# Kernel optimization log

Measured on AMD Instinct MI355X. Metric: run time of the kernel, lower is better.

Reference implementation:

```python
import jax, jax.numpy as jnp
import numpy as np

B, S, D_IN, D_OUT, RANK = 4, 2048, 4096, 4096, 32
BLOCK = 16
Q_MAX = 7.0  # INT4: 2**(4-1) - 1


def quantize_uniform(x, block_size=BLOCK, q_max=Q_MAX):
    """Block-wise symmetric fake-quantize (round-to-nearest, clamp)."""
    orig_shape = x.shape
    xf = x.reshape(-1, block_size)
    amax = jnp.clip(jnp.max(jnp.abs(xf), axis=-1, keepdims=True), 1e-12, None)
    scale = amax / q_max
    xq = jnp.clip(jnp.round(xf / scale), -q_max, q_max) * scale
    return xq.reshape(orig_shape)


def setup_inputs() -> dict:
    key = jax.random.key(0)
    ks = jax.random.split(key, 7)
    x = jax.random.normal(ks[0], (B, S, D_IN), jnp.float32)
    smooth_scale = jax.random.uniform(ks[1], (D_IN,), jnp.float32, 0.5, 2.0)
    w_quantized = jax.random.normal(ks[2], (D_OUT, D_IN), jnp.float32) * 0.02
    lora_a = jax.random.normal(ks[3], (RANK, D_IN), jnp.float32) * 0.02
    lora_b = jax.random.normal(ks[4], (D_OUT, RANK), jnp.float32) * 0.02
    w_sparse = jax.random.normal(ks[5], (D_OUT, D_IN), jnp.float32) * 0.02
    bias = jax.random.normal(ks[6], (D_OUT,), jnp.float32) * 0.02
    return {"x": x, "smooth_scale": smooth_scale, "w_quantized": w_quantized,
            "lora_a": lora_a, "lora_b": lora_b, "w_sparse": w_sparse, "bias": bias}


def reference(x, smooth_scale, w_quantized, lora_a, lora_b, w_sparse, bias):
    # smoothing (SmoothQuant-style per-channel scale)
    x_smoothed = x * smooth_scale                      # [B,S,Din]
    # block-wise INT4 fake-quantize of the smoothed activations
    x_q = quantize_uniform(x_smoothed)                 # [B,S,Din]
    # quantized main path
    base_out = jnp.einsum('bsi,oi->bso', x_q, w_quantized)
    # low-rank SVD error-correction path
    svd_out = jnp.einsum('bsr,or->bso',
                         jnp.einsum('bsi,ri->bsr', x_smoothed, lora_a),
                         lora_b)
    # sparse-outlier path (unsmoothed x)
    sparse_out = jnp.einsum('bsi,oi->bso', x, w_sparse)
    return base_out + svd_out + sparse_out + bias
```

## Files before the change

kernel.cpp:

```cpp
#include <hip/hip_runtime.h>
#include <stdint.h>

typedef float  f32x4  __attribute__((ext_vector_type(4)));
typedef __bf16 bf16x8 __attribute__((ext_vector_type(8)));
typedef unsigned int   u32;
typedef unsigned short u16;
typedef unsigned long long u64;
typedef u32 u32x4 __attribute__((ext_vector_type(4)));

#define M_TOT 8192
#define N_TOT 4096
#define K_DIN 4096
#define RANK  32
#define KCAT  8320
#define NTILE 130
#define KLAST 8256

__device__ __forceinline__ u16 f2bf(float f) {
  union { float f; u32 u; } v; v.f = f;
  u32 r = v.u + 0x7fffu + ((v.u >> 16) & 1u);
  return (u16)(r >> 16);
}

__global__ void prep_b_k(const float* __restrict__ wq, const float* __restrict__ wsp,
                         const float* __restrict__ lb, const float* __restrict__ la,
                         const float* __restrict__ ss,
                         u16* __restrict__ Bb, u16* __restrict__ asb) {
  const int b = blockIdx.x;
  const int tid = threadIdx.x;
  if (b < 32768) {
    const float* src = (b < 16384) ? wq : wsp;
    const int colofs = (b < 16384) ? 0 : K_DIN;
    const int i = (b & 16383) * 256 + tid;
    f32x4 v = ((const f32x4*)src)[i];
    int r = i >> 10, c = (i & 1023) * 4;
    alignas(8) u16 o[4] = { f2bf(v[0]), f2bf(v[1]), f2bf(v[2]), f2bf(v[3]) };
    *(u64*)(Bb + (size_t)r * KCAT + colofs + c) = *(const u64*)o;
  } else if (b < 32896) {
    const int i = (b - 32768) * 256 + tid;
    f32x4 v = ((const f32x4*)lb)[i];
    int row = i >> 3, c = (i & 7) * 4;
    alignas(8) u16 o[4] = { f2bf(v[0]), f2bf(v[1]), f2bf(v[2]), f2bf(v[3]) };
    u16* rp = Bb + (size_t)row * KCAT;
    *(u64*)(rp + 2 * K_DIN + c) = *(const u64*)o;
    u16* zp = rp + 2 * K_DIN + RANK + (i & 7) * 12;
    *(u64*)(zp + 0) = 0; *(u64*)(zp + 4) = 0; *(u64*)(zp + 8) = 0;
  } else {
    const int i = (b - 32896) * 256 + tid;
    f32x4 v = ((const f32x4*)la)[i];
    f32x4 s = ((const f32x4*)ss)[i & 1023];
    f32x4 p = v * s;
    alignas(8) u16 o[4] = { f2bf(p[0]), f2bf(p[1]), f2bf(p[2]), f2bf(p[3]) };
    *(u64*)(asb + 4 * (size_t)i) = *(const u64*)o;
  }
}

__global__ void prep_x_k(const float* __restrict__ x, const float* __restrict__ ss,
                         u16* __restrict__ Ab) {
  int m = blockIdx.x;
  int t = threadIdx.x;
  const f32x4* xp = (const f32x4*)(x + (size_t)m * K_DIN + t * 16);
  const f32x4* sp = (const f32x4*)(ss + t * 16);
  float xs[16];
  alignas(16) u16 rb[16], qb[16];
  float amax = 0.0f;
  #pragma unroll
  for (int i = 0; i < 4; ++i) {
    f32x4 a = xp[i], s = sp[i];
    #pragma unroll
    for (int j = 0; j < 4; ++j) {
      float xr = a[j];
      float v  = xr * s[j];
      xs[i*4+j] = v;
      amax = fmaxf(amax, fabsf(v));
      rb[i*4+j] = f2bf(xr);
    }
  }
  amax = fmaxf(amax, 1e-12f);
  float scale = amax / 7.0f;
  #pragma unroll
  for (int i = 0; i < 16; ++i) {
    float r = rintf(xs[i] / scale);
    r = fminf(7.0f, fmaxf(-7.0f, r));
    qb[i] = f2bf(r * scale);
  }
  u16* qo = Ab + (size_t)m * KCAT + t * 16;
  ((u32x4*)qo)[0] = ((const u32x4*)qb)[0];
  ((u32x4*)qo)[1] = ((const u32x4*)qb)[1];
  u16* ro = qo + K_DIN;
  ((u32x4*)ro)[0] = ((const u32x4*)rb)[0];
  ((u32x4*)ro)[1] = ((const u32x4*)rb)[1];
}

__global__ __launch_bounds__(256)
void lora_t_mfma_k(u16* __restrict__ Ab, const u16* __restrict__ asb) {
  const int wave = threadIdx.x >> 6;
  const int lane = threadIdx.x & 63;
  const int lr = lane & 15, lg = lane >> 4;
  const int m0 = blockIdx.x * 64 + wave * 16;
  f32x4 acc0 = {}, acc1 = {};
  for (int k0 = 0; k0 < K_DIN; k0 += 32) {
    bf16x8 a  = *(const bf16x8*)(Ab + (size_t)(m0 + lr) * KCAT + K_DIN + k0 + lg * 8);
    bf16x8 b0 = *(const bf16x8*)(asb + (size_t)lr        * K_DIN + k0 + lg * 8);
    bf16x8 b1 = *(const bf16x8*)(asb + (size_t)(16 + lr) * K_DIN + k0 + lg * 8);
    acc0 = __builtin_amdgcn_mfma_f32_16x16x32_bf16(a, b0, acc0, 0, 0, 0);
    acc1 = __builtin_amdgcn_mfma_f32_16x16x32_bf16(a, b1, acc1, 0, 0, 0);
  }
  #pragma unroll
  for (int j = 0; j < 4; ++j) {
    const int row = m0 + lg * 4 + j;
    Ab[(size_t)row * KCAT + 2 * K_DIN + lr]      = f2bf(acc0[j]);
    Ab[(size_t)row * KCAT + 2 * K_DIN + 16 + lr] = f2bf(acc1[j]);
  }
  const int zr = blockIdx.x * 64 + (threadIdx.x >> 2);
  u16* zp = Ab + (size_t)zr * KCAT + 2 * K_DIN + RANK + (threadIdx.x & 3) * 24;
  #pragma unroll
  for (int q = 0; q < 6; ++q) *(u64*)(zp + q * 4) = 0;
}

__device__ __forceinline__ void gld_lds16(const u16* g, u16* l) {
  __builtin_amdgcn_global_load_lds((const __attribute__((address_space(1))) u32*)g,
                                   (__attribute__((address_space(3))) u32*)l,
                                   16, 0, 0);
}

#define BAR()  __builtin_amdgcn_s_barrier()
#define VMW6() asm volatile("s_waitcnt vmcnt(6)" ::: "memory")
#define BUF1 32768

#define LDA(bufel, mh) do { _Pragma("unroll")                                        \
  for (int m_ = 0; m_ < 4; ++m_) {                                                   \
    Ar[m_][0] = *(const bf16x8*)(smem + (bufel) + aoff + ((mh)*4+m_)*1024 + blk0);    \
    Ar[m_][1] = *(const bf16x8*)(smem + (bufel) + aoff + ((mh)*4+m_)*1024 + blk1);    \
  } } while (0)

#define LDB(bufel, nh) do { _Pragma("unroll")                                        \
  for (int n_ = 0; n_ < 2; ++n_) {                                                   \
    Br[(nh)*2+n_][0] = *(const bf16x8*)(smem + (bufel) + boff + ((nh)*2+n_)*1024 + blk0); \
    Br[(nh)*2+n_][1] = *(const bf16x8*)(smem + (bufel) + boff + ((nh)*2+n_)*1024 + blk1); \
  } } while (0)

#define MMQ2(mh) do {                                                                \
  __builtin_amdgcn_s_setprio(1);                                                     \
  _Pragma("unroll")                                                                  \
  for (int m_ = 0; m_ < 4; ++m_) { _Pragma("unroll")                                 \
    for (int n_ = 0; n_ < 4; ++n_) {                                                 \
      acc[(mh)*4+m_][n_] = __builtin_amdgcn_mfma_f32_16x16x32_bf16(                  \
          Ar[m_][0], Br[n_][0], acc[(mh)*4+m_][n_], 0, 0, 0);                        \
      acc[(mh)*4+m_][n_] = __builtin_amdgcn_mfma_f32_16x16x32_bf16(                  \
          Ar[m_][1], Br[n_][1], acc[(mh)*4+m_][n_], 0, 0, 0);                        \
    } }                                                                              \
  __builtin_amdgcn_s_setprio(0);                                                     \
} while (0)

__global__ __launch_bounds__(512, 2)
void gemm8_k(const u16* __restrict__ Ab, const u16* __restrict__ Bb,
             const float* __restrict__ bias, float* __restrict__ out) {
  extern __shared__ u16 smem[];
  const int tid  = threadIdx.x;
  const int wave = tid >> 6;
  const int lane = tid & 63;
  const int lr = lane & 15, lg = lane >> 4;
  const int wm = wave >> 2, wn = wave & 3;

  const int wg  = blockIdx.x;
  const int swz = (wg & 7) * 64 + (wg >> 3);
  const int m0 = (swz >> 4) * 256;
  const int n0 = (swz & 15) * 256;

  const int aoff = wm * 8192 + lr * 64;
  const int boff = 16384 + wn * 4096 + lr * 64;
  const int e7   = lr & 7;
  const int blk0 = ((0 + lg) ^ e7) * 8;
  const int blk1 = ((4 + lg) ^ e7) * 8;

  const int srow = tid >> 3;
  const int scol = ((tid & 7) ^ (srow & 7)) * 8;
  const int woff = wave * 512;

  const u16* aRow = Ab + (size_t)(m0 + srow) * KCAT + scol;
  const u16* bRow = Bb + (size_t)(n0 + srow) * KCAT + scol;
  u16* dstA0 = smem + woff;
  u16* dstB0 = smem + 16384 + woff;

  bf16x8 Ar[4][2], Br[4][2];
  f32x4 acc[8][4] = {};

  auto stgA = [&](int kof, int h, int bufel) {
    u16* dst = dstA0 + bufel + h * 8192;
    gld_lds16(aRow + (size_t)(h * 128) * KCAT + kof, dst);
    gld_lds16(aRow + (size_t)(h * 128 + 64) * KCAT + kof, dst + 4096);
  };
  auto stgB = [&](int kof, int h, int bufel) {
    u16* dst = dstB0 + bufel + h * 8192;
    gld_lds16(bRow + (size_t)(h * 128) * KCAT + kof, dst);
    gld_lds16(bRow + (size_t)(h * 128 + 64) * KCAT + kof, dst + 4096);
  };

  stgA(0, 0, 0);     stgA(0, 1, 0);
  stgB(0, 0, 0);     stgB(0, 1, 0);
  stgB(64, 0, BUF1); stgB(64, 1, BUF1);
  stgA(64, 0, BUF1);
  VMW6();
  BAR();

  for (int it = 0; it < NTILE / 2; ++it) {
    const int ka = it * 128;
    int c2 = ka + 128, c3 = ka + 192;
    if (c2 > KLAST) c2 = KLAST;
    if (c3 > KLAST) c3 = KLAST;
    LDA(0, 0); LDB(0, 0); LDB(0, 1);
    stgA(ka + 64, 1, BUF1);
    BAR(); MMQ2(0); BAR();
    LDA(0, 1);
    stgB(c2, 0, 0); stgB(c2, 1, 0); stgA(c2, 0, 0);
    BAR(); MMQ2(1);
    VMW6();
    BAR();
    LDA(BUF1, 0); LDB(BUF1, 0); LDB(BUF1, 1);
    stgA(c2, 1, 0);
    BAR(); MMQ2(0); BAR();
    LDA(BUF1, 1);
    stgB(c3, 0, BUF1); stgB(c3, 1, BUF1); stgA(c3, 0, BUF1);
    BAR(); MMQ2(1);
    VMW6();
    BAR();
  }

  float bv[4];
  #pragma unroll
  for (int n = 0; n < 4; ++n) bv[n] = bias[n0 + wn * 64 + n * 16 + lr];
  #pragma unroll
  for (int m = 0; m < 8; ++m) {
    const int row = m0 + wm * 128 + m * 16 + lg * 4;
    #pragma unroll
    for (int n = 0; n < 4; ++n) {
      const int col = n0 + wn * 64 + n * 16 + lr;
      float* op = out + (size_t)row * N_TOT + col;
      op[0 * (size_t)N_TOT] = acc[m][n][0] + bv[n];
      op[1 * (size_t)N_TOT] = acc[m][n][1] + bv[n];
      op[2 * (size_t)N_TOT] = acc[m][n][2] + bv[n];
      op[3 * (size_t)N_TOT] = acc[m][n][3] + bv[n];
    }
  }
}

extern "C" void kernel_launch(void* const* d_in, const int* in_sizes, int n_in,
                              void* d_out, int out_size, void* d_ws, size_t ws_size,
                              hipStream_t stream) {
  const float* x    = (const float*)d_in[0];
  const float* ss   = (const float*)d_in[1];
  const float* wq   = (const float*)d_in[2];
  const float* la   = (const float*)d_in[3];
  const float* lb   = (const float*)d_in[4];
  const float* wsp  = (const float*)d_in[5];
  const float* bias = (const float*)d_in[6];
  float* out = (float*)d_out;

  uint8_t* w = (uint8_t*)d_ws;
  u16* Ab  = (u16*)w;  w += (size_t)M_TOT * KCAT * 2;
  u16* Bb  = (u16*)w;  w += (size_t)N_TOT * KCAT * 2;
  u16* asb = (u16*)w;

  prep_b_k<<<33024, 256, 0, stream>>>(wq, wsp, lb, la, ss, Bb, asb);
  prep_x_k<<<M_TOT, 256, 0, stream>>>(x, ss, Ab);
  lora_t_mfma_k<<<M_TOT / 64, 256, 0, stream>>>(Ab, asb);

  hipFuncSetAttribute((const void*)gemm8_k,
                      hipFuncAttributeMaxDynamicSharedMemorySize, 131072);
  gemm8_k<<<dim3((N_TOT / 256) * (M_TOT / 256)), 512, 131072, stream>>>(
      Ab, Bb, bias, out);
}
```

Baseline: 608.5 us.

## Split MFMA phases into quarter-tiles to interleave LDS reads and global stages

Splits each half-tile MFMA block into two quarter blocks indexed by n-half. The B fragment loads and global-to-LDS stages are spread between these finer phases, with the second m-half walked in reversed n order so the resident B registers are reused. The aim is better overlap of LDS reads and memory issue with matrix work in the ping-pong schedule. The cost is twice as many barriers per iteration, which may add synchronisation stalls.

```diff
diff --git a/kernel.cpp b/kernel.cpp
--- a/kernel.cpp
+++ b/kernel.cpp
@@ -140,15 +140,15 @@
     Br[(nh)*2+n_][1] = *(const bf16x8*)(smem + (bufel) + boff + ((nh)*2+n_)*1024 + blk1); \
   } } while (0)
 
-#define MMQ2(mh) do {                                                                \
+#define MMQ(mh, nh) do {                                                             \
   __builtin_amdgcn_s_setprio(1);                                                     \
   _Pragma("unroll")                                                                  \
   for (int m_ = 0; m_ < 4; ++m_) { _Pragma("unroll")                                 \
-    for (int n_ = 0; n_ < 4; ++n_) {                                                 \
-      acc[(mh)*4+m_][n_] = __builtin_amdgcn_mfma_f32_16x16x32_bf16(                  \
-          Ar[m_][0], Br[n_][0], acc[(mh)*4+m_][n_], 0, 0, 0);                        \
-      acc[(mh)*4+m_][n_] = __builtin_amdgcn_mfma_f32_16x16x32_bf16(                  \
-          Ar[m_][1], Br[n_][1], acc[(mh)*4+m_][n_], 0, 0, 0);                        \
+    for (int n_ = 0; n_ < 2; ++n_) {                                                 \
+      acc[(mh)*4+m_][(nh)*2+n_] = __builtin_amdgcn_mfma_f32_16x16x32_bf16(           \
+          Ar[m_][0], Br[(nh)*2+n_][0], acc[(mh)*4+m_][(nh)*2+n_], 0, 0, 0);          \
+      acc[(mh)*4+m_][(nh)*2+n_] = __builtin_amdgcn_mfma_f32_16x16x32_bf16(           \
+          Ar[m_][1], Br[(nh)*2+n_][1], acc[(mh)*4+m_][(nh)*2+n_], 0, 0, 0);          \
     } }                                                                              \
   __builtin_amdgcn_s_setprio(0);                                                     \
 } while (0)
@@ -209,20 +209,28 @@
     int c2 = ka + 128, c3 = ka + 192;
     if (c2 > KLAST) c2 = KLAST;
     if (c3 > KLAST) c3 = KLAST;
-    LDA(0, 0); LDB(0, 0); LDB(0, 1);
+    LDA(0, 0); LDB(0, 0);
     stgA(ka + 64, 1, BUF1);
-    BAR(); MMQ2(0); BAR();
+    BAR(); MMQ(0, 0); BAR();
+    LDB(0, 1);
+    BAR(); MMQ(0, 1); BAR();
     LDA(0, 1);
-    stgB(c2, 0, 0); stgB(c2, 1, 0); stgA(c2, 0, 0);
-    BAR(); MMQ2(1);
+    stgB(c2, 0, 0); stgB(c2, 1, 0);
+    BAR(); MMQ(1, 1); BAR();
+    stgA(c2, 0, 0);
+    BAR(); MMQ(1, 0);
     VMW6();
     BAR();
-    LDA(BUF1, 0); LDB(BUF1, 0); LDB(BUF1, 1);
+    LDA(BUF1, 0); LDB(BUF1, 0);
     stgA(c2, 1, 0);
-    BAR(); MMQ2(0); BAR();
+    BAR(); MMQ(0, 0); BAR();
+    LDB(BUF1, 1);
+    BAR(); MMQ(0, 1); BAR();
     LDA(BUF1, 1);
-    stgB(c3, 0, BUF1); stgB(c3, 1, BUF1); stgA(c3, 0, BUF1);
-    BAR(); MMQ2(1);
+    stgB(c3, 0, BUF1); stgB(c3, 1, BUF1);
+    BAR(); MMQ(1, 1); BAR();
+    stgA(c3, 0, BUF1);
+    BAR(); MMQ(1, 0);
     VMW6();
     BAR();
   }
```

Result: faster. 586.2 us (-3.7%).
